# Optimization experiments

Measured on AMD Instinct MI355X. Metric: run time of the kernel, lower is better.

Reference implementation:

```python
import jax, jax.numpy as jnp
import numpy as np

K_HOPS = 2  # number_layers


def _gcn_norm(edge_index, edge_weight, num_nodes):
    # add self loops with weight 1 (PyG gcn_norm default, fill_value=1)
    row, col = edge_index[0], edge_index[1]
    loop = jnp.arange(num_nodes, dtype=edge_index.dtype)
    row = jnp.concatenate([row, loop])
    col = jnp.concatenate([col, loop])
    w = jnp.concatenate([edge_weight, jnp.ones((num_nodes,), edge_weight.dtype)])
    deg = jax.ops.segment_sum(w, col, num_segments=num_nodes)
    dinv = jnp.where(deg > 0, jax.lax.rsqrt(deg), 0.0)
    norm = dinv[row] * w * dinv[col]
    return row, col, norm


def setup_inputs() -> dict:
    key = jax.random.key(0)
    k1, k2, k3, k4 = jax.random.split(key, 4)
    N, E, F_IN, F_OUT = 100000, 1600000, 256, 40
    x = jax.random.normal(k1, (N, F_IN), dtype=jnp.float32)
    edge_index = jax.random.randint(k2, (2, E), 0, N, dtype=jnp.int64)
    edge_attr = jax.random.uniform(k3, (E,), dtype=jnp.float32)
    W = jax.random.normal(k4, (F_OUT, F_IN), dtype=jnp.float32) * (1.0 / np.sqrt(F_IN))
    b = jnp.zeros((F_OUT,), dtype=jnp.float32)
    return {"x": x, "edge_index": edge_index, "edge_attr": edge_attr, "W": W, "b": b}


def reference(x, edge_index, edge_attr, W, b):
    N = x.shape[0]
    row, col, norm = _gcn_norm(edge_index, edge_attr, N)
    for _ in range(K_HOPS):
        x = jax.ops.segment_sum(norm[:, None] * x[row], col, num_segments=N)
    out = x @ W.T + b           # SGConv final linear
    out = jax.nn.relu(out)      # dropout is a no-op in eval mode
    return jax.nn.log_softmax(out, axis=-1)
```

## Files before the change

### kernel.cpp

```cpp
#include <hip/hip_runtime.h>
#include <hip/hip_bf16.h>
#include <math.h>

#define TF_IN   256
#define TF_OUT  40
#define NCH2    5
#define BCAP    48
#define WQ      32767.0f
#define BIN_SHIFT 6
#define MAXBINS 1600
#define EPB 4096
#define BINCAP 1280


struct us8 { ushort4 a, b; };

__device__ inline float bf2f(unsigned short u) {
    union { unsigned int i; float f; } t; t.i = ((unsigned int)u) << 16; return t.f;
}
__device__ inline unsigned short f2bf(float f) {
    union { float f; unsigned int i; } t; t.f = f;
    unsigned int r = t.i + 0x7FFF + ((t.i >> 16) & 1);
    return (unsigned short)(r >> 16);
}

__device__ inline void acc8(float* acc, float v, const us8& h) {
    acc[0] += v * bf2f(h.a.x); acc[1] += v * bf2f(h.a.y);
    acc[2] += v * bf2f(h.a.z); acc[3] += v * bf2f(h.a.w);
    acc[4] += v * bf2f(h.b.x); acc[5] += v * bf2f(h.b.y);
    acc[6] += v * bf2f(h.b.z); acc[7] += v * bf2f(h.b.w);
}

__global__ void zero_kernel(int* __restrict__ a, int na) {
    int i = blockIdx.x * blockDim.x + threadIdx.x;
    if (i < na) a[i] = 0;
}

struct PartSh { int hist[MAXBINS]; unsigned int cursor[MAXBINS]; };
struct GemmSh { float4 xs[128][8]; float4 wsm[40][9]; };
union FusedSh { PartSh p; GemmSh g; };

__global__ __launch_bounds__(256) void fused_part_gemm_kernel(
        const float* __restrict__ x, const float* __restrict__ W,
        unsigned short* __restrict__ h, int N, int partBlocks,
        const int* __restrict__ row, const int* __restrict__ col,
        const float* __restrict__ w, int E,
        int* __restrict__ binCnt, uint2* __restrict__ bins, int nbins) {
    __shared__ FusedSh sh;
    int tid = threadIdx.x;

    if ((int)blockIdx.x < partBlocks) {
        int base = (int)blockIdx.x * EPB;
        for (int i = tid; i < nbins; i += 256) sh.p.hist[i] = 0;

        int   ec[16], er[16];
        float ev[16];
#pragma unroll
        for (int i = 0; i < 16; ++i) ec[i] = -1;
#pragma unroll
        for (int q = 0; q < 4; ++q) {
            int e = base + (q * 256 + tid) * 4;
            if (e + 4 <= E) {
                int4   c4 = *(const int4*)(col + e);
                int4   r4 = *(const int4*)(row + e);
                float4 w4 = *(const float4*)(w + e);
                ec[q * 4 + 0] = c4.x; ec[q * 4 + 1] = c4.y; ec[q * 4 + 2] = c4.z; ec[q * 4 + 3] = c4.w;
                er[q * 4 + 0] = r4.x; er[q * 4 + 1] = r4.y; er[q * 4 + 2] = r4.z; er[q * 4 + 3] = r4.w;
                ev[q * 4 + 0] = w4.x; ev[q * 4 + 1] = w4.y; ev[q * 4 + 2] = w4.z; ev[q * 4 + 3] = w4.w;
            } else {
                for (int j = 0; j < 4; ++j) {
                    int ee = e + j;
                    if (ee < E) { ec[q * 4 + j] = col[ee]; er[q * 4 + j] = row[ee]; ev[q * 4 + j] = w[ee]; }
                }
            }
        }
        __syncthreads();

#pragma unroll
        for (int i = 0; i < 16; ++i)
            if (ec[i] >= 0) atomicAdd(&sh.p.hist[ec[i] >> BIN_SHIFT], 1);
        __syncthreads();

        for (int bq = tid; bq < nbins; bq += 256) {
            int hc = sh.p.hist[bq];
            unsigned int g = (unsigned int)bq * (unsigned int)BINCAP;
            if (hc > 0) g += (unsigned int)atomicAdd(&binCnt[bq], hc);
            sh.p.cursor[bq] = g;
        }
        __syncthreads();

#pragma unroll
        for (int i = 0; i < 16; ++i) {
            if (ec[i] >= 0) {
                int bq = ec[i] >> BIN_SHIFT;
                unsigned int p = atomicAdd(&sh.p.cursor[bq], 1u);
                if (p < (unsigned int)(bq + 1) * (unsigned int)BINCAP) {
                    unsigned int wq = (unsigned int)(ev[i] * WQ + 0.5f);
                    uint2 ent; ent.x = ((unsigned int)er[i] << 15) | wq; ent.y = (unsigned int)ec[i];
                    bins[p] = ent;
                }
            }
        }
    } else {
        int q = (int)blockIdx.x - partBlocks;
        int ng = tid >> 2;
        int jg = tid & 3;
        int j0 = jg * 10;
        int nodeBase = q * 128;
        int sk = (ng >> 1) & 7;

        float acc[2][10];
#pragma unroll
        for (int i = 0; i < 2; ++i)
#pragma unroll
            for (int j = 0; j < 10; ++j) acc[i][j] = 0.f;

        const float4* x4 = (const float4*)x;
        const float4* W4 = (const float4*)W;

        float4 px[4], pw0, pw1;
        int xn[4], xc[4];
#pragma unroll
        for (int i = 0; i < 4; ++i) {
            int idx = tid + i * 256;
            xn[i] = idx >> 3; xc[i] = idx & 7;
        }
        int wj0 = tid >> 3, wc0 = tid & 7;
        int wj1 = (tid + 256) >> 3, wc1 = (tid + 256) & 7;

#pragma unroll
        for (int i = 0; i < 4; ++i) {
            int gn = nodeBase + xn[i];
            px[i] = (gn < N) ? x4[(size_t)gn * (TF_IN / 4) + xc[i]]
                             : make_float4(0.f, 0.f, 0.f, 0.f);
        }
        pw0 = W4[(size_t)wj0 * (TF_IN / 4) + wc0];
        if (tid < 64) pw1 = W4[(size_t)wj1 * (TF_IN / 4) + wc1];

        for (int kt = 0; kt < 8; ++kt) {
            __syncthreads();
#pragma unroll
            for (int i = 0; i < 4; ++i)
                sh.g.xs[xn[i]][xc[i] ^ ((xn[i] >> 2) & 7)] = px[i];
            sh.g.wsm[wj0][wc0] = pw0;
            if (tid < 64) sh.g.wsm[wj1][wc1] = pw1;
            __syncthreads();

            if (kt < 7) {
                int kb4n = (kt + 1) * 8;
#pragma unroll
                for (int i = 0; i < 4; ++i) {
                    int gn = nodeBase + xn[i];
                    px[i] = (gn < N) ? x4[(size_t)gn * (TF_IN / 4) + kb4n + xc[i]]
                                     : make_float4(0.f, 0.f, 0.f, 0.f);
                }
                pw0 = W4[(size_t)wj0 * (TF_IN / 4) + kb4n + wc0];
                if (tid < 64) pw1 = W4[(size_t)wj1 * (TF_IN / 4) + kb4n + wc1];
            }

#pragma unroll 2
            for (int c4 = 0; c4 < 8; ++c4) {
                int phys = c4 ^ sk;
                float4 xv0 = sh.g.xs[ng * 2][phys];
                float4 xv1 = sh.g.xs[ng * 2 + 1][phys];
#pragma unroll
                for (int jj = 0; jj < 10; ++jj) {
                    float4 wv = sh.g.wsm[j0 + jj][c4];
                    acc[0][jj] += xv0.x * wv.x + xv0.y * wv.y + xv0.z * wv.z + xv0.w * wv.w;
                    acc[1][jj] += xv1.x * wv.x + xv1.y * wv.y + xv1.z * wv.z + xv1.w * wv.w;
                }
            }
        }

#pragma unroll
        for (int i = 0; i < 2; ++i) {
            int gn = nodeBase + ng * 2 + i;
            if (gn < N) {
                ushort2* hp2 = (ushort2*)(h + (size_t)gn * TF_OUT + j0);
#pragma unroll
                for (int p = 0; p < 5; ++p) {
                    ushort2 o;
                    o.x = f2bf(acc[i][2 * p]);
                    o.y = f2bf(acc[i][2 * p + 1]);
                    hp2[p] = o;
                }
            }
        }
    }
}

__global__ __launch_bounds__(256) void deg_bin_kernel(
        const uint2* __restrict__ bins, const int* __restrict__ binCnt,
        float* __restrict__ dinv, int N) {
    __shared__ int wsumi[64];
    int tid = threadIdx.x;
    int b = blockIdx.x;
    if (tid < 64) wsumi[tid] = 0;
    __syncthreads();

    int mb = binCnt[b]; if (mb > BINCAP) mb = BINCAP;
    const uint2* src = bins + (size_t)b * BINCAP;
    for (int i = tid; i < mb; i += 256) {
        uint2 e = src[i];
        atomicAdd(&wsumi[e.y & 63], (int)(e.x & 0x7FFF));
    }
    __syncthreads();

    if (tid < 64) {
        int node = b * 64 + tid;
        if (node < N)
            dinv[node] = rsqrtf(1.0f + (float)wsumi[tid] * (1.0f / WQ));
    }
}

__device__ inline void stage_bin(int tid, int mb, const uint2* __restrict__ src,
                                 const float* __restrict__ dinv,
                                 int* lcnt, int rs[64][BCAP + 1], float vs[64][BCAP + 1]) {
    for (int i = tid; i < mb; i += 320) {
        uint2 e = src[i];
        int r = (int)(e.x >> 15);
        float v = dinv[r] * ((float)(e.x & 0x7FFF) * (1.0f / WQ));
        int g2 = (int)(e.y & 63u);
        int pos = atomicAdd(&lcnt[g2], 1);
        if (pos < BCAP) { rs[g2][pos] = r; vs[g2][pos] = v; }
    }
}

__device__ inline void gather_lds(float* acc, const us8* __restrict__ hin,
                                  int g, int chunk, int m,
                                  const int rs[64][BCAP + 1], const float vs[64][BCAP + 1]) {
    int k = 0;
    for (; k + 8 <= m; k += 8) {
        us8 h0 = hin[(size_t)rs[g][k + 0] * NCH2 + chunk];
        us8 h1 = hin[(size_t)rs[g][k + 1] * NCH2 + chunk];
        us8 h2 = hin[(size_t)rs[g][k + 2] * NCH2 + chunk];
        us8 h3 = hin[(size_t)rs[g][k + 3] * NCH2 + chunk];
        us8 h4 = hin[(size_t)rs[g][k + 4] * NCH2 + chunk];
        us8 h5 = hin[(size_t)rs[g][k + 5] * NCH2 + chunk];
        us8 h6 = hin[(size_t)rs[g][k + 6] * NCH2 + chunk];
        us8 h7 = hin[(size_t)rs[g][k + 7] * NCH2 + chunk];
        acc8(acc, vs[g][k + 0], h0); acc8(acc, vs[g][k + 1], h1);
        acc8(acc, vs[g][k + 2], h2); acc8(acc, vs[g][k + 3], h3);
        acc8(acc, vs[g][k + 4], h4); acc8(acc, vs[g][k + 5], h5);
        acc8(acc, vs[g][k + 6], h6); acc8(acc, vs[g][k + 7], h7);
    }
    if (k + 4 <= m) {
        us8 h0 = hin[(size_t)rs[g][k + 0] * NCH2 + chunk];
        us8 h1 = hin[(size_t)rs[g][k + 1] * NCH2 + chunk];
        us8 h2 = hin[(size_t)rs[g][k + 2] * NCH2 + chunk];
        us8 h3 = hin[(size_t)rs[g][k + 3] * NCH2 + chunk];
        acc8(acc, vs[g][k + 0], h0); acc8(acc, vs[g][k + 1], h1);
        acc8(acc, vs[g][k + 2], h2); acc8(acc, vs[g][k + 3], h3);
        k += 4;
    }
    for (; k < m; ++k) {
        us8 hv = hin[(size_t)rs[g][k] * NCH2 + chunk];
        acc8(acc, vs[g][k], hv);
    }
}

__global__ __launch_bounds__(320) void hop1_kernel(
        const us8* __restrict__ hin, us8* __restrict__ hout,
        const uint2* __restrict__ bins, const int* __restrict__ binCnt,
        const float* __restrict__ dinv, int N) {
    __shared__ int   rs[64][BCAP + 1];
    __shared__ float vs[64][BCAP + 1];
    __shared__ int   lcnt[64];
    int tid = threadIdx.x;
    int b = blockIdx.x;
    int g = tid / NCH2;
    int chunk = tid - g * NCH2;
    int node = b * 64 + g;

    if (tid < 64) lcnt[tid] = 0;
    __syncthreads();

    int mb = binCnt[b]; if (mb > BINCAP) mb = BINCAP;
    stage_bin(tid, mb, bins + (size_t)b * BINCAP, dinv, lcnt, rs, vs);
    __syncthreads();
    if (node >= N) return;

    float d = dinv[node];
    int m = lcnt[g]; if (m > BCAP) m = BCAP;

    us8 a = hin[(size_t)node * NCH2 + chunk];
    float acc[8];
    acc[0] = bf2f(a.a.x) * d; acc[1] = bf2f(a.a.y) * d;
    acc[2] = bf2f(a.a.z) * d; acc[3] = bf2f(a.a.w) * d;
    acc[4] = bf2f(a.b.x) * d; acc[5] = bf2f(a.b.y) * d;
    acc[6] = bf2f(a.b.z) * d; acc[7] = bf2f(a.b.w) * d;

    gather_lds(acc, hin, g, chunk, m, rs, vs);

    us8 o;
    o.a.x = f2bf(acc[0] * d); o.a.y = f2bf(acc[1] * d);
    o.a.z = f2bf(acc[2] * d); o.a.w = f2bf(acc[3] * d);
    o.b.x = f2bf(acc[4] * d); o.b.y = f2bf(acc[5] * d);
    o.b.z = f2bf(acc[6] * d); o.b.w = f2bf(acc[7] * d);
    hout[(size_t)node * NCH2 + chunk] = o;
}

__global__ __launch_bounds__(320) void hop2_epi_kernel(
        const us8* __restrict__ hin, float4* __restrict__ out,
        const uint2* __restrict__ bins, const int* __restrict__ binCnt,
        const float* __restrict__ dinv, const float* __restrict__ bias, int N) {
    __shared__ int   rs[64][BCAP + 1];
    __shared__ float vs[64][BCAP + 1];
    __shared__ int   lcnt[64];
    __shared__ float redm[320];
    __shared__ float reds[320];
    int tid = threadIdx.x;
    int b = blockIdx.x;
    int g = tid / NCH2;
    int chunk = tid - g * NCH2;
    int node = b * 64 + g;
    bool valid = node < N;

    if (tid < 64) lcnt[tid] = 0;
    __syncthreads();

    int mb = binCnt[b]; if (mb > BINCAP) mb = BINCAP;
    stage_bin(tid, mb, bins + (size_t)b * BINCAP, dinv, lcnt, rs, vs);
    __syncthreads();

    float acc[8];
#pragma unroll
    for (int j = 0; j < 8; ++j) acc[j] = 0.f;
    float d = 0.f;
    if (valid) {
        d = dinv[node];
        int m = lcnt[g]; if (m > BCAP) m = BCAP;
        us8 a = hin[(size_t)node * NCH2 + chunk];
        acc[0] = bf2f(a.a.x) * d; acc[1] = bf2f(a.a.y) * d;
        acc[2] = bf2f(a.a.z) * d; acc[3] = bf2f(a.a.w) * d;
        acc[4] = bf2f(a.b.x) * d; acc[5] = bf2f(a.b.y) * d;
        acc[6] = bf2f(a.b.z) * d; acc[7] = bf2f(a.b.w) * d;
        gather_lds(acc, hin, g, chunk, m, rs, vs);
    }

    float v[8];
    float lm = -1e30f;
    if (valid) {
#pragma unroll
        for (int j = 0; j < 8; ++j) {
            float t2 = acc[j] * d + bias[chunk * 8 + j];
            t2 = fmaxf(t2, 0.f);
            v[j] = t2;
            lm = fmaxf(lm, t2);
        }
    }
    redm[tid] = lm;
    __syncthreads();
    float gm = redm[g * NCH2];
#pragma unroll
    for (int i = 1; i < NCH2; ++i) gm = fmaxf(gm, redm[g * NCH2 + i]);

    float ps = 0.f;
    if (valid) {
#pragma unroll
        for (int j = 0; j < 8; ++j) ps += __expf(v[j] - gm);
    }
    reds[tid] = ps;
    __syncthreads();
    float s = reds[g * NCH2];
#pragma unroll
    for (int i = 1; i < NCH2; ++i) s += reds[g * NCH2 + i];
    float lse = gm + __logf(s);

    if (valid) {
        float4 o0 = make_float4(v[0] - lse, v[1] - lse, v[2] - lse, v[3] - lse);
        float4 o1 = make_float4(v[4] - lse, v[5] - lse, v[6] - lse, v[7] - lse);
        out[(size_t)node * 10 + chunk * 2]     = o0;
        out[(size_t)node * 10 + chunk * 2 + 1] = o1;
    }
}

extern "C" void kernel_launch(void* const* d_in, const int* in_sizes, int n_in,
                              void* d_out, int out_size, void* d_ws, size_t ws_size,
                              hipStream_t stream) {
    const float* x  = (const float*)d_in[0];
    const int*   ei = (const int*)d_in[1];
    const float* ew = (const float*)d_in[2];
    const float* W  = (const float*)d_in[3];
    const float* b  = (const float*)d_in[4];

    const int F_out = in_sizes[4];
    const int F_in  = in_sizes[3] / F_out;
    const int N     = in_sizes[0] / F_in;
    const int E     = in_sizes[2];
    const int* row = ei;
    const int* col = ei + E;

    char* ws = (char*)d_ws;
    size_t off = 0;
    auto alloc = [&](size_t bytes) {
        void* p = ws + off;
        off += (bytes + 255) & ~(size_t)255;
        return p;
    };

    int nbins = (N + (1 << BIN_SHIFT) - 1) >> BIN_SHIFT;

    float*        dinv   = (float*)        alloc((size_t)N * 4);
    uint2*        bins   = (uint2*)        alloc((size_t)nbins * BINCAP * 8);
    unsigned short* h0   = (unsigned short*)alloc((size_t)N * TF_OUT * 2);
    unsigned short* h1   = (unsigned short*)alloc((size_t)N * TF_OUT * 2);
    int*          binCnt = (int*)          alloc((size_t)nbins * 4);

    const int tb = 256;
    hipLaunchKernelGGL(zero_kernel, dim3((nbins + tb - 1) / tb), dim3(tb), 0, stream,
                       binCnt, nbins);

    int partBlocks = (E + EPB - 1) / EPB;
    int gemmBlocks = (N + 127) / 128;
    hipLaunchKernelGGL(fused_part_gemm_kernel, dim3(partBlocks + gemmBlocks), dim3(256),
                       0, stream, x, W, h0, N, partBlocks, row, col, ew, E,
                       binCnt, bins, nbins);

    hipLaunchKernelGGL(deg_bin_kernel, dim3(nbins), dim3(256), 0, stream,
                       bins, binCnt, dinv, N);

    hipLaunchKernelGGL(hop1_kernel, dim3(nbins), dim3(320), 0, stream,
                       (const us8*)h0, (us8*)h1, bins, binCnt, dinv, N);

    hipLaunchKernelGGL(hop2_epi_kernel, dim3(nbins), dim3(320), 0, stream,
                       (const us8*)h1, (float4*)d_out, bins, binCnt, dinv, b, N);
}
```

Before: 292.1 us.

## Switch hidden features to planar layout and gather per plane in passes

The GEMM now writes bf16 features in a plane-major layout: five planes of 8 features, each plane holding all N nodes contiguously. A new finalize kernel precomputes the per-edge normalized value and packs the source row with the local slot, so each hop block no longer looks up dinv while staging. Each hop is split into three launches covering 2, 2 and 1 planes, so each gather pass touches a smaller working set (N×16 bytes per plane) that may fit in cache better. The log-softmax epilogue moves to a separate kernel that reads the fp32 hop-2 output back from memory. The cost is more launches, repeated bin staging in every pass, and an extra round trip through the output buffer.

```diff
diff --git a/kernel.cpp b/kernel.cpp
--- a/kernel.cpp
+++ b/kernel.cpp
@@ -4,7 +4,6 @@
 
 #define TF_IN   256
 #define TF_OUT  40
-#define NCH2    5
 #define BCAP    48
 #define WQ      32767.0f
 #define BIN_SHIFT 6
@@ -176,13 +175,14 @@
         for (int i = 0; i < 2; ++i) {
             int gn = nodeBase + ng * 2 + i;
             if (gn < N) {
-                ushort2* hp2 = (ushort2*)(h + (size_t)gn * TF_OUT + j0);
 #pragma unroll
                 for (int p = 0; p < 5; ++p) {
+                    int j = j0 + 2 * p;
+                    int plane = j >> 3, off = j & 7;
                     ushort2 o;
                     o.x = f2bf(acc[i][2 * p]);
                     o.y = f2bf(acc[i][2 * p + 1]);
-                    hp2[p] = o;
+                    *(ushort2*)(h + ((size_t)plane * N + gn) * 8 + off) = o;
                 }
             }
         }
@@ -213,165 +213,138 @@
     }
 }
 
-__device__ inline void stage_bin(int tid, int mb, const uint2* __restrict__ src,
-                                 const float* __restrict__ dinv,
-                                 int* lcnt, int rs[64][BCAP + 1], float vs[64][BCAP + 1]) {
-    for (int i = tid; i < mb; i += 320) {
+__global__ __launch_bounds__(256) void finalize_kernel(
+        uint2* __restrict__ bins, const int* __restrict__ binCnt,
+        const float* __restrict__ dinv) {
+    int tid = threadIdx.x;
+    int b = blockIdx.x;
+    int mb = binCnt[b]; if (mb > BINCAP) mb = BINCAP;
+    uint2* src = bins + (size_t)b * BINCAP;
+    for (int i = tid; i < mb; i += 256) {
         uint2 e = src[i];
-        int r = (int)(e.x >> 15);
+        unsigned int r = e.x >> 15;
         float v = dinv[r] * ((float)(e.x & 0x7FFF) * (1.0f / WQ));
-        int g2 = (int)(e.y & 63u);
-        int pos = atomicAdd(&lcnt[g2], 1);
-        if (pos < BCAP) { rs[g2][pos] = r; vs[g2][pos] = v; }
-    }
-}
-
-__device__ inline void gather_lds(float* acc, const us8* __restrict__ hin,
-                                  int g, int chunk, int m,
-                                  const int rs[64][BCAP + 1], const float vs[64][BCAP + 1]) {
+        uint2 ne;
+        ne.x = (r << 6) | (e.y & 63u);
+        ne.y = __float_as_uint(v);
+        src[i] = ne;
+    }
+}
+
+__device__ inline void gather_plane(float* acc, const us8* __restrict__ hp,
+                                    int g, int m,
+                                    const int rs[64][BCAP + 1], const float vs[64][BCAP + 1]) {
     int k = 0;
     for (; k + 8 <= m; k += 8) {
-        us8 h0 = hin[(size_t)rs[g][k + 0] * NCH2 + chunk];
-        us8 h1 = hin[(size_t)rs[g][k + 1] * NCH2 + chunk];
-        us8 h2 = hin[(size_t)rs[g][k + 2] * NCH2 + chunk];
-        us8 h3 = hin[(size_t)rs[g][k + 3] * NCH2 + chunk];
-        us8 h4 = hin[(size_t)rs[g][k + 4] * NCH2 + chunk];
-        us8 h5 = hin[(size_t)rs[g][k + 5] * NCH2 + chunk];
-        us8 h6 = hin[(size_t)rs[g][k + 6] * NCH2 + chunk];
-        us8 h7 = hin[(size_t)rs[g][k + 7] * NCH2 + chunk];
+        us8 h0 = hp[rs[g][k + 0]]; us8 h1 = hp[rs[g][k + 1]];
+        us8 h2 = hp[rs[g][k + 2]]; us8 h3 = hp[rs[g][k + 3]];
+        us8 h4 = hp[rs[g][k + 4]]; us8 h5 = hp[rs[g][k + 5]];
+        us8 h6 = hp[rs[g][k + 6]]; us8 h7 = hp[rs[g][k + 7]];
         acc8(acc, vs[g][k + 0], h0); acc8(acc, vs[g][k + 1], h1);
         acc8(acc, vs[g][k + 2], h2); acc8(acc, vs[g][k + 3], h3);
         acc8(acc, vs[g][k + 4], h4); acc8(acc, vs[g][k + 5], h5);
         acc8(acc, vs[g][k + 6], h6); acc8(acc, vs[g][k + 7], h7);
     }
     if (k + 4 <= m) {
-        us8 h0 = hin[(size_t)rs[g][k + 0] * NCH2 + chunk];
-        us8 h1 = hin[(size_t)rs[g][k + 1] * NCH2 + chunk];
-        us8 h2 = hin[(size_t)rs[g][k + 2] * NCH2 + chunk];
-        us8 h3 = hin[(size_t)rs[g][k + 3] * NCH2 + chunk];
+        us8 h0 = hp[rs[g][k + 0]]; us8 h1 = hp[rs[g][k + 1]];
+        us8 h2 = hp[rs[g][k + 2]]; us8 h3 = hp[rs[g][k + 3]];
         acc8(acc, vs[g][k + 0], h0); acc8(acc, vs[g][k + 1], h1);
         acc8(acc, vs[g][k + 2], h2); acc8(acc, vs[g][k + 3], h3);
         k += 4;
     }
-    for (; k < m; ++k) {
-        us8 hv = hin[(size_t)rs[g][k] * NCH2 + chunk];
-        acc8(acc, vs[g][k], hv);
-    }
-}
-
-__global__ __launch_bounds__(320) void hop1_kernel(
-        const us8* __restrict__ hin, us8* __restrict__ hout,
+    for (; k < m; ++k) { us8 hv = hp[rs[g][k]]; acc8(acc, vs[g][k], hv); }
+}
+
+template<bool F32OUT>
+__global__ __launch_bounds__(128) void hop_pass_kernel(
+        const us8* __restrict__ hin, us8* __restrict__ hout, float* __restrict__ fout,
         const uint2* __restrict__ bins, const int* __restrict__ binCnt,
-        const float* __restrict__ dinv, int N) {
+        const float* __restrict__ dinv, int N, int plane_lo, int nplanes) {
     __shared__ int   rs[64][BCAP + 1];
     __shared__ float vs[64][BCAP + 1];
     __shared__ int   lcnt[64];
     int tid = threadIdx.x;
     int b = blockIdx.x;
-    int g = tid / NCH2;
-    int chunk = tid - g * NCH2;
-    int node = b * 64 + g;
 
     if (tid < 64) lcnt[tid] = 0;
     __syncthreads();
 
     int mb = binCnt[b]; if (mb > BINCAP) mb = BINCAP;
-    stage_bin(tid, mb, bins + (size_t)b * BINCAP, dinv, lcnt, rs, vs);
+    const uint2* src = bins + (size_t)b * BINCAP;
+    for (int i = tid; i < mb; i += 128) {
+        uint2 e = src[i];
+        int g2 = (int)(e.x & 63u);
+        int pos = atomicAdd(&lcnt[g2], 1);
+        if (pos < BCAP) {
+            rs[g2][pos] = (int)(e.x >> 6);
+            vs[g2][pos] = __uint_as_float(e.y);
+        }
+    }
     __syncthreads();
+
+    if (tid >= 64 * nplanes) return;
+    int g = tid & 63;
+    int p = plane_lo + (tid >> 6);
+    int node = b * 64 + g;
     if (node >= N) return;
 
     float d = dinv[node];
     int m = lcnt[g]; if (m > BCAP) m = BCAP;
-
-    us8 a = hin[(size_t)node * NCH2 + chunk];
+    const us8* hp = hin + (size_t)p * N;
+
+    us8 a = hp[node];
     float acc[8];
     acc[0] = bf2f(a.a.x) * d; acc[1] = bf2f(a.a.y) * d;
     acc[2] = bf2f(a.a.z) * d; acc[3] = bf2f(a.a.w) * d;
     acc[4] = bf2f(a.b.x) * d; acc[5] = bf2f(a.b.y) * d;
     acc[6] = bf2f(a.b.z) * d; acc[7] = bf2f(a.b.w) * d;
 
-    gather_lds(acc, hin, g, chunk, m, rs, vs);
-
-    us8 o;
-    o.a.x = f2bf(acc[0] * d); o.a.y = f2bf(acc[1] * d);
-    o.a.z = f2bf(acc[2] * d); o.a.w = f2bf(acc[3] * d);
-    o.b.x = f2bf(acc[4] * d); o.b.y = f2bf(acc[5] * d);
-    o.b.z = f2bf(acc[6] * d); o.b.w = f2bf(acc[7] * d);
-    hout[(size_t)node * NCH2 + chunk] = o;
-}
-
-__global__ __launch_bounds__(320) void hop2_epi_kernel(
-        const us8* __restrict__ hin, float4* __restrict__ out,
-        const uint2* __restrict__ bins, const int* __restrict__ binCnt,
-        const float* __restrict__ dinv, const float* __restrict__ bias, int N) {
-    __shared__ int   rs[64][BCAP + 1];
-    __shared__ float vs[64][BCAP + 1];
-    __shared__ int   lcnt[64];
-    __shared__ float redm[320];
-    __shared__ float reds[320];
-    int tid = threadIdx.x;
-    int b = blockIdx.x;
-    int g = tid / NCH2;
-    int chunk = tid - g * NCH2;
-    int node = b * 64 + g;
-    bool valid = node < N;
-
-    if (tid < 64) lcnt[tid] = 0;
-    __syncthreads();
-
-    int mb = binCnt[b]; if (mb > BINCAP) mb = BINCAP;
-    stage_bin(tid, mb, bins + (size_t)b * BINCAP, dinv, lcnt, rs, vs);
-    __syncthreads();
-
-    float acc[8];
-#pragma unroll
-    for (int j = 0; j < 8; ++j) acc[j] = 0.f;
-    float d = 0.f;
-    if (valid) {
-        d = dinv[node];
-        int m = lcnt[g]; if (m > BCAP) m = BCAP;
-        us8 a = hin[(size_t)node * NCH2 + chunk];
-        acc[0] = bf2f(a.a.x) * d; acc[1] = bf2f(a.a.y) * d;
-        acc[2] = bf2f(a.a.z) * d; acc[3] = bf2f(a.a.w) * d;
-        acc[4] = bf2f(a.b.x) * d; acc[5] = bf2f(a.b.y) * d;
-        acc[6] = bf2f(a.b.z) * d; acc[7] = bf2f(a.b.w) * d;
-        gather_lds(acc, hin, g, chunk, m, rs, vs);
-    }
-
-    float v[8];
-    float lm = -1e30f;
-    if (valid) {
-#pragma unroll
-        for (int j = 0; j < 8; ++j) {
-            float t2 = acc[j] * d + bias[chunk * 8 + j];
-            t2 = fmaxf(t2, 0.f);
-            v[j] = t2;
-            lm = fmaxf(lm, t2);
-        }
-    }
-    redm[tid] = lm;
-    __syncthreads();
-    float gm = redm[g * NCH2];
-#pragma unroll
-    for (int i = 1; i < NCH2; ++i) gm = fmaxf(gm, redm[g * NCH2 + i]);
-
-    float ps = 0.f;
-    if (valid) {
-#pragma unroll
-        for (int j = 0; j < 8; ++j) ps += __expf(v[j] - gm);
-    }
-    reds[tid] = ps;
-    __syncthreads();
-    float s = reds[g * NCH2];
-#pragma unroll
-    for (int i = 1; i < NCH2; ++i) s += reds[g * NCH2 + i];
-    float lse = gm + __logf(s);
-
-    if (valid) {
-        float4 o0 = make_float4(v[0] - lse, v[1] - lse, v[2] - lse, v[3] - lse);
-        float4 o1 = make_float4(v[4] - lse, v[5] - lse, v[6] - lse, v[7] - lse);
-        out[(size_t)node * 10 + chunk * 2]     = o0;
-        out[(size_t)node * 10 + chunk * 2 + 1] = o1;
+    gather_plane(acc, hp, g, m, rs, vs);
+
+    if (F32OUT) {
+        float4* o4 = (float4*)(fout + (size_t)node * TF_OUT + 8 * p);
+        o4[0] = make_float4(acc[0] * d, acc[1] * d, acc[2] * d, acc[3] * d);
+        o4[1] = make_float4(acc[4] * d, acc[5] * d, acc[6] * d, acc[7] * d);
+    } else {
+        us8 o;
+        o.a.x = f2bf(acc[0] * d); o.a.y = f2bf(acc[1] * d);
+        o.a.z = f2bf(acc[2] * d); o.a.w = f2bf(acc[3] * d);
+        o.b.x = f2bf(acc[4] * d); o.b.y = f2bf(acc[5] * d);
+        o.b.z = f2bf(acc[6] * d); o.b.w = f2bf(acc[7] * d);
+        hout[(size_t)p * N + node] = o;
+    }
+}
+
+__global__ void epilogue_kernel(float* __restrict__ out, const float* __restrict__ b, int N) {
+    int n = blockIdx.x * blockDim.x + threadIdx.x;
+    if (n >= N) return;
+    float4* o4 = (float4*)out + (size_t)n * (TF_OUT / 4);
+    float v[TF_OUT];
+#pragma unroll
+    for (int i = 0; i < TF_OUT / 4; ++i) {
+        float4 t = o4[i];
+        v[4 * i] = t.x; v[4 * i + 1] = t.y; v[4 * i + 2] = t.z; v[4 * i + 3] = t.w;
+    }
+    float m = -1e30f;
+#pragma unroll
+    for (int j = 0; j < TF_OUT; ++j) {
+        float t = v[j] + b[j];
+        t = fmaxf(t, 0.f);
+        v[j] = t;
+        m = fmaxf(m, t);
+    }
+    float s = 0.f;
+#pragma unroll
+    for (int j = 0; j < TF_OUT; ++j) s += __expf(v[j] - m);
+    float lse = m + __logf(s);
+#pragma unroll
+    for (int i = 0; i < TF_OUT / 4; ++i) {
+        float4 t;
+        t.x = v[4 * i]     - lse;
+        t.y = v[4 * i + 1] - lse;
+        t.z = v[4 * i + 2] - lse;
+        t.w = v[4 * i + 3] - lse;
+        o4[i] = t;
     }
 }
 
@@ -420,9 +393,23 @@
     hipLaunchKernelGGL(deg_bin_kernel, dim3(nbins), dim3(256), 0, stream,
                        bins, binCnt, dinv, N);
 
-    hipLaunchKernelGGL(hop1_kernel, dim3(nbins), dim3(320), 0, stream,
-                       (const us8*)h0, (us8*)h1, bins, binCnt, dinv, N);
-
-    hipLaunchKernelGGL(hop2_epi_kernel, dim3(nbins), dim3(320), 0, stream,
-                       (const us8*)h1, (float4*)d_out, bins, binCnt, dinv, b, N);
-}
+    hipLaunchKernelGGL(finalize_kernel, dim3(nbins), dim3(256), 0, stream,
+                       bins, binCnt, dinv);
+
+    hipLaunchKernelGGL((hop_pass_kernel<false>), dim3(nbins), dim3(128), 0, stream,
+                       (const us8*)h0, (us8*)h1, (float*)nullptr, bins, binCnt, dinv, N, 0, 2);
+    hipLaunchKernelGGL((hop_pass_kernel<false>), dim3(nbins), dim3(128), 0, stream,
+                       (const us8*)h0, (us8*)h1, (float*)nullptr, bins, binCnt, dinv, N, 2, 2);
+    hipLaunchKernelGGL((hop_pass_kernel<false>), dim3(nbins), dim3(128), 0, stream,
+                       (const us8*)h0, (us8*)h1, (float*)nullptr, bins, binCnt, dinv, N, 4, 1);
+
+    hipLaunchKernelGGL((hop_pass_kernel<true>), dim3(nbins), dim3(128), 0, stream,
+                       (const us8*)h1, (us8*)nullptr, (float*)d_out, bins, binCnt, dinv, N, 0, 2);
+    hipLaunchKernelGGL((hop_pass_kernel<true>), dim3(nbins), dim3(128), 0, stream,
+                       (const us8*)h1, (us8*)nullptr, (float*)d_out, bins, binCnt, dinv, N, 2, 2);
+    hipLaunchKernelGGL((hop_pass_kernel<true>), dim3(nbins), dim3(128), 0, stream,
+                       (const us8*)h1, (us8*)nullptr, (float*)d_out, bins, binCnt, dinv, N, 4, 1);
+
+    hipLaunchKernelGGL(epilogue_kernel, dim3((N + tb - 1) / tb), dim3(tb), 0, stream,
+                       (float*)d_out, b, N);
+}
```

After: 377.2 us. +29.1%, slower.
